# Kernel tuning notes

Hardware: AMD Instinct MI355X
Metric: run time of the kernel (lower is better)

The kernel has to match this reference:

```python
import jax, jax.numpy as jnp
import numpy as np

OUT, IN, RANK = 4096, 4096, 512
B, S = 4, 2048


def setup_inputs() -> dict:
    key = jax.random.key(0)
    k_x, k_qa, k_qb, k_sa, k_sb, k_b = jax.random.split(key, 6)
    x = jax.random.normal(k_x, (B, S, IN), dtype=jnp.float32)
    # int8-style symmetric quantized CP factors (stored as int32 for the harness)
    q_a = jax.random.randint(k_qa, (OUT, RANK), -127, 127, dtype=jnp.int32)
    q_b = jax.random.randint(k_qb, (IN, RANK), -127, 127, dtype=jnp.int32)
    scale_a = jax.random.uniform(k_sa, (), dtype=jnp.float32) * 0.01 + 1e-4
    scale_b = jax.random.uniform(k_sb, (), dtype=jnp.float32) * 0.01 + 1e-4
    bias = jax.random.normal(k_b, (OUT,), dtype=jnp.float32)
    return {"x": x, "q_a": q_a, "q_b": q_b, "scale_a": scale_a,
            "scale_b": scale_b, "bias": bias}


def reference(x, q_a, q_b, scale_a, scale_b, bias):
    # dequantize_factors(): symmetric per-factor dequant q * scale
    a = q_a.astype(jnp.float32) * scale_a          # [OUT, RANK]
    b = q_b.astype(jnp.float32) * scale_b          # [IN,  RANK]
    # CP reconstruction: weight = factors[0] @ factors[1].T, viewed as [OUT, IN]
    weight = a @ b.T                               # [OUT, IN] (materialized, as in original)
    # F.linear(x, weight, bias) = x @ weight.T + bias
    return jnp.einsum('bsi,oi->bso', x, weight) + bias
```

## Files before the change

kernel.cpp:

```cpp
#include <hip/hip_runtime.h>
#include <hip/hip_fp16.h>


#define M_TOT 8192
#define N_OUT 4096
#define K_IN  4096
#define RANK  512

typedef _Float16 f16x8 __attribute__((ext_vector_type(8)));
typedef float f32x4 __attribute__((ext_vector_type(4)));

#define WAIT_VM0() asm volatile("s_waitcnt vmcnt(0)" ::: "memory")
#define WAIT_VM8() asm volatile("s_waitcnt vmcnt(8)" ::: "memory")
#define BARRIER() do { __builtin_amdgcn_s_barrier(); __builtin_amdgcn_sched_barrier(0); } while (0)

__device__ __forceinline__ void gload_lds16(const void* g, void* l) {
  __builtin_amdgcn_global_load_lds(
      (const __attribute__((address_space(1))) unsigned int*)g,
      (__attribute__((address_space(3))) unsigned int*)l, 16, 0, 0);
}

__global__ void k_cvt_x(const float4* __restrict__ X, uint4* __restrict__ O, int n8) {
  int i = blockIdx.x * blockDim.x + threadIdx.x;
  if (i >= n8) return;
  float4 a = X[2 * i], b = X[2 * i + 1];
  uint4 r;
  __half2* h = (__half2*)&r;
  h[0] = __floats2half2_rn(a.x, a.y);
  h[1] = __floats2half2_rn(a.z, a.w);
  h[2] = __floats2half2_rn(b.x, b.y);
  h[3] = __floats2half2_rn(b.z, b.w);
  O[i] = r;
}

__global__ void k_cvt_qa(const int4* __restrict__ q, ushort4* __restrict__ o, int n4) {
  int i = blockIdx.x * blockDim.x + threadIdx.x;
  if (i >= n4) return;
  int4 v = q[i];
  ushort4 r;
  r.x = __half_as_ushort(__float2half_rn((float)v.x));
  r.y = __half_as_ushort(__float2half_rn((float)v.y));
  r.z = __half_as_ushort(__float2half_rn((float)v.z));
  r.w = __half_as_ushort(__float2half_rn((float)v.w));
  o[i] = r;
}

__global__ void k_transpose_qb(const int* __restrict__ qb, __half* __restrict__ qbt) {
  __shared__ __half tile[32][33];
  int tx = threadIdx.x & 31, ty = threadIdx.x >> 5;
  int k0 = blockIdx.x * 32, r0 = blockIdx.y * 32;
#pragma unroll
  for (int j = 0; j < 4; ++j)
    tile[ty + j * 8][tx] = __float2half_rn((float)qb[(size_t)(k0 + ty + j * 8) * RANK + r0 + tx]);
  __syncthreads();
#pragma unroll
  for (int j = 0; j < 4; ++j)
    qbt[(size_t)(r0 + ty + j * 8) * K_IN + k0 + tx] = tile[tx][ty + j * 8];
}

__global__ __launch_bounds__(256, 2) void k_gemm1p(
    const __half* __restrict__ XH, const __half* __restrict__ Bt,
    __half* __restrict__ P) {
  __shared__ __align__(16) uint4 lds[2][2048];
  const int tid = threadIdx.x;
  const int lane = tid & 63, wid = tid >> 6, wm = wid & 1, wn = wid >> 1;
  const int blk = blockIdx.x;
  const int xcd = blk & 7, local = blk >> 3;
  const int z = xcd >> 1;
  const int n_t = (xcd & 1) * 2 + (local & 1);
  const int m_t = local >> 1;
  const int m0 = m_t * 128, n0 = n_t * 128;
  const int kbeg = z * (K_IN / 4);
  const int fr = lane & 15, fq = lane >> 4;

  f32x4 acc[4][4] = {};

  auto stage = [&](int kt, int buf) {
#pragma unroll
    for (int c = 0; c < 4; ++c) {
      int d = tid + 256 * c;
      int r = d >> 3, s = (d & 7) ^ (r & 7);
      gload_lds16(XH + (size_t)(m0 + r) * K_IN + kbeg + kt * 64 + s * 8, &lds[buf][d]);
    }
#pragma unroll
    for (int c = 0; c < 4; ++c) {
      int d = tid + 256 * c;
      int r = d >> 3, s = (d & 7) ^ (r & 7);
      gload_lds16(Bt + (size_t)(n0 + r) * K_IN + kbeg + kt * 64 + s * 8, &lds[buf][1024 + d]);
    }
  };

  stage(0, 0);
  stage(1, 1);
  WAIT_VM8();
  BARRIER();

  const int NT = (K_IN / 4) / 64;
  for (int t = 0; t < NT; ++t) {
    const int cur = t & 1;
#pragma unroll
    for (int kk = 0; kk < 2; ++kk) {
      int s = kk * 4 + fq;
      f16x8 a[4], b[4];
#pragma unroll
      for (int mi = 0; mi < 4; ++mi) {
        int r = wm * 64 + mi * 16 + fr;
        a[mi] = *(const f16x8*)&lds[cur][r * 8 + (s ^ (r & 7))];
      }
#pragma unroll
      for (int ni = 0; ni < 4; ++ni) {
        int n = wn * 64 + ni * 16 + fr;
        b[ni] = *(const f16x8*)&lds[cur][1024 + n * 8 + (s ^ (n & 7))];
      }
#pragma unroll
      for (int mi = 0; mi < 4; ++mi)
#pragma unroll
        for (int ni = 0; ni < 4; ++ni)
          acc[mi][ni] = __builtin_amdgcn_mfma_f32_16x16x32_f16(a[mi], b[ni], acc[mi][ni], 0, 0, 0);
    }
    if (t == NT - 1) break;
    BARRIER();
    if (t + 2 < NT) {
      stage(t + 2, cur);
      WAIT_VM8();
    } else {
      WAIT_VM0();
    }
    BARRIER();
  }

  __half* Pz = P + (size_t)z * M_TOT * RANK;
#pragma unroll
  for (int mi = 0; mi < 4; ++mi)
#pragma unroll
    for (int ni = 0; ni < 4; ++ni) {
      int col = n0 + wn * 64 + ni * 16 + fr;
      int rbase = m0 + wm * 64 + mi * 16 + fq * 4;
#pragma unroll
      for (int j = 0; j < 4; ++j)
        Pz[(size_t)(rbase + j) * RANK + col] = __float2half_rn(acc[mi][ni][j]);
    }
}

__global__ __launch_bounds__(256, 4) void k_gemm1_fb(
    const float* __restrict__ X, const __half* __restrict__ Bt,
    __half* __restrict__ P) {
  __shared__ __align__(16) uint4 lds[2560];
  const int tid = threadIdx.x;
  const int lane = tid & 63, wn = tid >> 6;
  const int flat = blockIdx.x;
  const int xcd = flat & 7, local = flat >> 3;
  const int z = xcd >> 1;
  const int m_t = (xcd & 1) * 64 + (local >> 1);
  const int n_t = local & 1;
  const int m0 = m_t * 64, n0 = n_t * 256;
  const int kbeg = z * (K_IN / 4);
  const int fr = lane & 15, fq = lane >> 4;

  f32x4 acc[4][4] = {};
  const int ar = tid >> 2, aq = tid & 3;
  const float* xbase = X + (size_t)(m0 + ar) * K_IN + aq * 16;
  const int aslot0 = ar * 8 + ((2 * aq) ^ (ar & 7));
  const int aslot1 = ar * 8 + ((2 * aq + 1) ^ (ar & 7));

  for (int it = 0; it < (K_IN / 4) / 64; ++it) {
    const int k0 = kbeg + it * 64;
#pragma unroll
    for (int c = 0; c < 8; ++c) {
      int d = tid + 256 * c;
      int r = d >> 3, s = (d & 7) ^ (r & 7);
      gload_lds16(Bt + (size_t)(n0 + r) * K_IN + k0 + s * 8, &lds[512 + d]);
    }
    float4 v0 = *(const float4*)(xbase + k0);
    float4 v1 = *(const float4*)(xbase + k0 + 4);
    float4 v2 = *(const float4*)(xbase + k0 + 8);
    float4 v3 = *(const float4*)(xbase + k0 + 12);
    union { __half2 h[4]; uint4 u; } p0, p1;
    p0.h[0] = __floats2half2_rn(v0.x, v0.y);
    p0.h[1] = __floats2half2_rn(v0.z, v0.w);
    p0.h[2] = __floats2half2_rn(v1.x, v1.y);
    p0.h[3] = __floats2half2_rn(v1.z, v1.w);
    p1.h[0] = __floats2half2_rn(v2.x, v2.y);
    p1.h[1] = __floats2half2_rn(v2.z, v2.w);
    p1.h[2] = __floats2half2_rn(v3.x, v3.y);
    p1.h[3] = __floats2half2_rn(v3.z, v3.w);
    lds[aslot0] = p0.u;
    lds[aslot1] = p1.u;
    __syncthreads();
#pragma unroll
    for (int kk = 0; kk < 2; ++kk) {
      const int s = kk * 4 + fq;
      f16x8 a[4], b[4];
#pragma unroll
      for (int mi = 0; mi < 4; ++mi) {
        int r = mi * 16 + fr;
        a[mi] = *(const f16x8*)&lds[r * 8 + (s ^ (r & 7))];
      }
#pragma unroll
      for (int ni = 0; ni < 4; ++ni) {
        int n = wn * 64 + ni * 16 + fr;
        b[ni] = *(const f16x8*)&lds[512 + n * 8 + (s ^ (n & 7))];
      }
#pragma unroll
      for (int mi = 0; mi < 4; ++mi)
#pragma unroll
        for (int ni = 0; ni < 4; ++ni)
          acc[mi][ni] = __builtin_amdgcn_mfma_f32_16x16x32_f16(a[mi], b[ni], acc[mi][ni], 0, 0, 0);
    }
    __syncthreads();
  }

  __half* Pz = P + (size_t)z * M_TOT * RANK;
#pragma unroll
  for (int mi = 0; mi < 4; ++mi)
#pragma unroll
    for (int ni = 0; ni < 4; ++ni) {
      int col = n0 + wn * 64 + ni * 16 + fr;
      int rbase = m0 + mi * 16 + fq * 4;
#pragma unroll
      for (int j = 0; j < 4; ++j)
        Pz[(size_t)(rbase + j) * RANK + col] = __float2half_rn(acc[mi][ni][j]);
    }
}

__global__ void k_reduce_t(const uint4* __restrict__ P, uint4* __restrict__ T8, int n8) {
  int i = blockIdx.x * blockDim.x + threadIdx.x;
  if (i >= n8) return;
  float2 f[4] = {};
#pragma unroll
  for (int zz = 0; zz < 4; ++zz) {
    uint4 v = P[(size_t)zz * n8 + i];
    const __half2* h = (const __half2*)&v;
#pragma unroll
    for (int j = 0; j < 4; ++j) {
      float2 g = __half22float2(h[j]);
      f[j].x += g.x; f[j].y += g.y;
    }
  }
  uint4 r;
  __half2* o = (__half2*)&r;
#pragma unroll
  for (int j = 0; j < 4; ++j) o[j] = __floats2half2_rn(f[j].x, f[j].y);
  T8[i] = r;
}

__global__ __launch_bounds__(256, 2) void k_gemm2(
    const __half* __restrict__ T, const __half* __restrict__ QA,
    const float* __restrict__ sa, const float* __restrict__ sb,
    const float* __restrict__ bias, float* __restrict__ Out) {
  __shared__ __align__(16) uint4 lds[2][2048];
  const int tid = threadIdx.x;
  const int lane = tid & 63, wid = tid >> 6, wm = wid & 1, wn = wid >> 1;
  const int flat = blockIdx.x;
  const int xcd = flat & 7, local = flat >> 3;
  const int n_t = xcd * 4 + (local & 3);
  const int m_t = local >> 2;
  const int m0 = m_t * 128, n0 = n_t * 128;
  const int fr = lane & 15, fq = lane >> 4;

  f32x4 acc[4][4] = {};

  auto stage = [&](int kt, int buf) {
#pragma unroll
    for (int c = 0; c < 4; ++c) {
      int d = tid + 256 * c;
      int r = d >> 3, s = (d & 7) ^ (r & 7);
      gload_lds16(T + (size_t)(m0 + r) * RANK + kt * 64 + s * 8, &lds[buf][d]);
    }
#pragma unroll
    for (int c = 0; c < 4; ++c) {
      int d = tid + 256 * c;
      int r = d >> 3, s = (d & 7) ^ (r & 7);
      gload_lds16(QA + (size_t)(n0 + r) * RANK + kt * 64 + s * 8, &lds[buf][1024 + d]);
    }
  };

  stage(0, 0);
  stage(1, 1);
  WAIT_VM8();
  BARRIER();

  const int NT = RANK / 64;
  for (int t = 0; t < NT; ++t) {
    const int cur = t & 1;
#pragma unroll
    for (int kk = 0; kk < 2; ++kk) {
      int s = kk * 4 + fq;
      f16x8 a[4], b[4];
#pragma unroll
      for (int mi = 0; mi < 4; ++mi) {
        int r = wm * 64 + mi * 16 + fr;
        a[mi] = *(const f16x8*)&lds[cur][r * 8 + (s ^ (r & 7))];
      }
#pragma unroll
      for (int ni = 0; ni < 4; ++ni) {
        int n = wn * 64 + ni * 16 + fr;
        b[ni] = *(const f16x8*)&lds[cur][1024 + n * 8 + (s ^ (n & 7))];
      }
#pragma unroll
      for (int mi = 0; mi < 4; ++mi)
#pragma unroll
        for (int ni = 0; ni < 4; ++ni)
          acc[mi][ni] = __builtin_amdgcn_mfma_f32_16x16x32_f16(a[mi], b[ni], acc[mi][ni], 0, 0, 0);
    }
    if (t == NT - 1) break;
    BARRIER();
    if (t + 2 < NT) {
      stage(t + 2, cur);
      WAIT_VM8();
    } else {
      WAIT_VM0();
    }
    BARRIER();
  }

  const float scale = sa[0] * sb[0];
#pragma unroll
  for (int mi = 0; mi < 4; ++mi)
#pragma unroll
    for (int ni = 0; ni < 4; ++ni) {
      int col = n0 + wn * 64 + ni * 16 + fr;
      float bv = bias[col];
      int rbase = m0 + wm * 64 + mi * 16 + fq * 4;
#pragma unroll
      for (int j = 0; j < 4; ++j)
        Out[(size_t)(rbase + j) * N_OUT + col] = acc[mi][ni][j] * scale + bv;
    }
}

extern "C" void kernel_launch(void* const* d_in, const int* in_sizes, int n_in,
                              void* d_out, int out_size, void* d_ws, size_t ws_size,
                              hipStream_t stream) {
  const float* x    = (const float*)d_in[0];
  const int*   qa   = (const int*)d_in[1];
  const int*   qb   = (const int*)d_in[2];
  const float* sa   = (const float*)d_in[3];
  const float* sb   = (const float*)d_in[4];
  const float* bias = (const float*)d_in[5];
  float* out = (float*)d_out;

  char* ws = (char*)d_ws;
  __half* qa_h = (__half*)ws;
  __half* qbt  = (__half*)(ws + (4u << 20));
  __half* t    = (__half*)(ws + (8u << 20));
  __half* part = (__half*)(ws + (16u << 20));
  __half* x_h  = (__half*)(ws + (48u << 20));

  k_cvt_qa<<<2048, 256, 0, stream>>>((const int4*)qa, (ushort4*)qa_h, (N_OUT * RANK) / 4);
  dim3 tg(K_IN / 32, RANK / 32);
  k_transpose_qb<<<tg, 256, 0, stream>>>(qb, qbt);

  const bool big_ws = ws_size >= (112ull << 20);
  if (big_ws) {
    const int nx8 = M_TOT * K_IN / 8;
    k_cvt_x<<<nx8 / 256, 256, 0, stream>>>((const float4*)x, (uint4*)x_h, nx8);
    k_gemm1p<<<1024, 256, 0, stream>>>(x_h, qbt, part);
  } else {
    k_gemm1_fb<<<1024, 256, 0, stream>>>(x, qbt, part);
  }
  const int n8 = M_TOT * RANK / 8;
  k_reduce_t<<<n8 / 256, 256, 0, stream>>>((const uint4*)part, (uint4*)t, n8);

  k_gemm2<<<2048, 256, 0, stream>>>(t, qa_h, sa, sb, bias, out);
}
```

Before: 141.9 us.

## Fuse fp32-to-fp16 conversion of x into first GEMM, use 512-thread 128x256 tiles

```diff
diff --git a/kernel.cpp b/kernel.cpp
--- a/kernel.cpp
+++ b/kernel.cpp
@@ -11,6 +11,7 @@
 typedef float f32x4 __attribute__((ext_vector_type(4)));
 
 #define WAIT_VM0() asm volatile("s_waitcnt vmcnt(0)" ::: "memory")
+#define WAIT_VM4() asm volatile("s_waitcnt vmcnt(4)" ::: "memory")
 #define WAIT_VM8() asm volatile("s_waitcnt vmcnt(8)" ::: "memory")
 #define BARRIER() do { __builtin_amdgcn_s_barrier(); __builtin_amdgcn_sched_barrier(0); } while (0)
 
@@ -18,19 +19,6 @@
   __builtin_amdgcn_global_load_lds(
       (const __attribute__((address_space(1))) unsigned int*)g,
       (__attribute__((address_space(3))) unsigned int*)l, 16, 0, 0);
-}
-
-__global__ void k_cvt_x(const float4* __restrict__ X, uint4* __restrict__ O, int n8) {
-  int i = blockIdx.x * blockDim.x + threadIdx.x;
-  if (i >= n8) return;
-  float4 a = X[2 * i], b = X[2 * i + 1];
-  uint4 r;
-  __half2* h = (__half2*)&r;
-  h[0] = __floats2half2_rn(a.x, a.y);
-  h[1] = __floats2half2_rn(a.z, a.w);
-  h[2] = __floats2half2_rn(b.x, b.y);
-  h[3] = __floats2half2_rn(b.z, b.w);
-  O[i] = r;
 }
 
 __global__ void k_cvt_qa(const int4* __restrict__ q, ushort4* __restrict__ o, int n4) {
@@ -58,18 +46,17 @@
     qbt[(size_t)(r0 + ty + j * 8) * K_IN + k0 + tx] = tile[tx][ty + j * 8];
 }
 
-__global__ __launch_bounds__(256, 2) void k_gemm1p(
-    const __half* __restrict__ XH, const __half* __restrict__ Bt,
+__global__ __launch_bounds__(512, 4) void k_gemm1v(
+    const float* __restrict__ X, const __half* __restrict__ Bt,
     __half* __restrict__ P) {
   __shared__ __align__(16) uint4 lds[2][2048];
   const int tid = threadIdx.x;
-  const int lane = tid & 63, wid = tid >> 6, wm = wid & 1, wn = wid >> 1;
+  const int lane = tid & 63, wid = tid >> 6;
+  const int wm = wid & 1, wn = wid >> 1;
   const int blk = blockIdx.x;
-  const int xcd = blk & 7, local = blk >> 3;
-  const int z = xcd >> 1;
-  const int n_t = (xcd & 1) * 2 + (local & 1);
-  const int m_t = local >> 1;
-  const int m0 = m_t * 128, n0 = n_t * 128;
+  const int xcd = blk & 7, m_t = blk >> 3;
+  const int z = xcd >> 1, n_t = xcd & 1;
+  const int m0 = m_t * 128, n0 = n_t * 256;
   const int kbeg = z * (K_IN / 4);
   const int fr = lane & 15, fq = lane >> 4;
 
@@ -77,52 +64,59 @@
 
   auto stage = [&](int kt, int buf) {
 #pragma unroll
-    for (int c = 0; c < 4; ++c) {
-      int d = tid + 256 * c;
+    for (int c = 0; c < 2; ++c) {
+      int d = tid + 512 * c;
       int r = d >> 3, s = (d & 7) ^ (r & 7);
-      gload_lds16(XH + (size_t)(m0 + r) * K_IN + kbeg + kt * 64 + s * 8, &lds[buf][d]);
-    }
-#pragma unroll
-    for (int c = 0; c < 4; ++c) {
-      int d = tid + 256 * c;
-      int r = d >> 3, s = (d & 7) ^ (r & 7);
-      gload_lds16(Bt + (size_t)(n0 + r) * K_IN + kbeg + kt * 64 + s * 8, &lds[buf][1024 + d]);
+      gload_lds16(X + (size_t)(m0 + r) * K_IN + kbeg + kt * 32 + s * 4, &lds[buf][d]);
+    }
+#pragma unroll
+    for (int c = 0; c < 2; ++c) {
+      int d = tid + 512 * c;
+      int p = d >> 3, u = (d & 7) ^ (p & 7);
+      gload_lds16(Bt + (size_t)(n0 + 2 * p + (u >> 2)) * K_IN + kbeg + kt * 32 + (u & 3) * 8,
+                  &lds[buf][1024 + d]);
     }
   };
 
   stage(0, 0);
   stage(1, 1);
-  WAIT_VM8();
+  WAIT_VM4();
   BARRIER();
 
-  const int NT = (K_IN / 4) / 64;
+  const int NT = (K_IN / 4) / 32;
   for (int t = 0; t < NT; ++t) {
-    const int cur = t & 1;
-#pragma unroll
-    for (int kk = 0; kk < 2; ++kk) {
-      int s = kk * 4 + fq;
-      f16x8 a[4], b[4];
-#pragma unroll
-      for (int mi = 0; mi < 4; ++mi) {
-        int r = wm * 64 + mi * 16 + fr;
-        a[mi] = *(const f16x8*)&lds[cur][r * 8 + (s ^ (r & 7))];
-      }
-#pragma unroll
-      for (int ni = 0; ni < 4; ++ni) {
-        int n = wn * 64 + ni * 16 + fr;
-        b[ni] = *(const f16x8*)&lds[cur][1024 + n * 8 + (s ^ (n & 7))];
-      }
-#pragma unroll
-      for (int mi = 0; mi < 4; ++mi)
-#pragma unroll
-        for (int ni = 0; ni < 4; ++ni)
-          acc[mi][ni] = __builtin_amdgcn_mfma_f32_16x16x32_f16(a[mi], b[ni], acc[mi][ni], 0, 0, 0);
-    }
+    const uint4* Ab = &lds[t & 1][0];
+    const uint4* Bb = &lds[t & 1][1024];
+    f16x8 a[4], b[4];
+#pragma unroll
+    for (int mi = 0; mi < 4; ++mi) {
+      int r = wm * 64 + mi * 16 + fr;
+      f32x4 u0 = *(const f32x4*)&Ab[r * 8 + ((fq * 2) ^ (r & 7))];
+      f32x4 u1 = *(const f32x4*)&Ab[r * 8 + ((fq * 2 + 1) ^ (r & 7))];
+      union { __half2 h[4]; f16x8 v; } pa;
+      pa.h[0] = __floats2half2_rn(u0[0], u0[1]);
+      pa.h[1] = __floats2half2_rn(u0[2], u0[3]);
+      pa.h[2] = __floats2half2_rn(u1[0], u1[1]);
+      pa.h[3] = __floats2half2_rn(u1[2], u1[3]);
+      a[mi] = pa.v;
+    }
+#pragma unroll
+    for (int ni = 0; ni < 4; ++ni) {
+      int r = wn * 64 + ni * 16 + fr;
+      int p = r >> 1;
+      b[ni] = *(const f16x8*)&Bb[p * 8 + ((((r & 1) << 2) | fq) ^ (p & 7))];
+    }
+#pragma unroll
+    for (int mi = 0; mi < 4; ++mi)
+#pragma unroll
+      for (int ni = 0; ni < 4; ++ni)
+        acc[mi][ni] = __builtin_amdgcn_mfma_f32_16x16x32_f16(a[mi], b[ni], acc[mi][ni], 0, 0, 0);
+
     if (t == NT - 1) break;
     BARRIER();
     if (t + 2 < NT) {
-      stage(t + 2, cur);
-      WAIT_VM8();
+      stage(t + 2, t & 1);
+      WAIT_VM4();
     } else {
       WAIT_VM0();
     }
@@ -344,20 +338,13 @@
   __half* qbt  = (__half*)(ws + (4u << 20));
   __half* t    = (__half*)(ws + (8u << 20));
   __half* part = (__half*)(ws + (16u << 20));
-  __half* x_h  = (__half*)(ws + (48u << 20));
 
   k_cvt_qa<<<2048, 256, 0, stream>>>((const int4*)qa, (ushort4*)qa_h, (N_OUT * RANK) / 4);
   dim3 tg(K_IN / 32, RANK / 32);
   k_transpose_qb<<<tg, 256, 0, stream>>>(qb, qbt);
 
-  const bool big_ws = ws_size >= (112ull << 20);
-  if (big_ws) {
-    const int nx8 = M_TOT * K_IN / 8;
-    k_cvt_x<<<nx8 / 256, 256, 0, stream>>>((const float4*)x, (uint4*)x_h, nx8);
-    k_gemm1p<<<1024, 256, 0, stream>>>(x_h, qbt, part);
-  } else {
-    k_gemm1_fb<<<1024, 256, 0, stream>>>(x, qbt, part);
-  }
+  k_gemm1v<<<512, 512, 0, stream>>>(x, qbt, part);
+
   const int n8 = M_TOT * RANK / 8;
   k_reduce_t<<<n8 / 256, 256, 0, stream>>>((const uint4*)part, (uint4*)t, n8);
 
```

Measured after the change: 133.2 us. -6.2%, faster.
